# Kernel tuning notes

Measured on AMD Instinct MI355X. Metric: run time of the kernel, lower is better.

## Reference

```python
import jax, jax.numpy as jnp
import numpy as np

N = 50000      # nodes
E = 800000     # edges (before self-loops)
H = 4          # attention heads
C = 32         # out_features per head
DIN = 128      # in_features (== H*C so residual path is active)
ED = 16        # edge_dim
NEG = 0.2      # LeakyReLU negative slope (GATConv default)
EPS = 1e-5     # LayerNorm eps


def setup_inputs() -> dict:
    key = jax.random.key(0)
    ks = jax.random.split(key, 12)
    s = 0.05
    return {
        "x": jax.random.normal(ks[0], (N, DIN), dtype=jnp.float32),
        "edge_index": jax.random.randint(ks[1], (2, E), 0, N, dtype=jnp.int64),
        "edge_attr": jax.random.normal(ks[2], (E, ED), dtype=jnp.float32),
        # edge_processor: Linear(ED, ED) + ReLU (dropout = identity at eval)
        "W_ep": jax.random.normal(ks[3], (ED, ED), dtype=jnp.float32) * s,
        "b_ep": jnp.zeros((ED,), dtype=jnp.float32),
        # GATConv params (lin / lin_edge are bias-free in PyG)
        "W_lin": jax.random.normal(ks[4], (DIN, H * C), dtype=jnp.float32) * s,
        "W_edge": jax.random.normal(ks[5], (ED, H * C), dtype=jnp.float32) * s,
        "att_src": jax.random.normal(ks[6], (H, C), dtype=jnp.float32) * s,
        "att_dst": jax.random.normal(ks[7], (H, C), dtype=jnp.float32) * s,
        "att_edge": jax.random.normal(ks[8], (H, C), dtype=jnp.float32) * s,
        "bias": jnp.zeros((H * C,), dtype=jnp.float32),
        # LayerNorm params
        "ln_g": jnp.ones((H * C,), dtype=jnp.float32),
        "ln_b": jnp.zeros((H * C,), dtype=jnp.float32),
    }


def reference(x, edge_index, edge_attr, W_ep, b_ep, W_lin, W_edge,
              att_src, att_dst, att_edge, bias, ln_g, ln_b):
    n = x.shape[0]
    src, dst = edge_index[0], edge_index[1]

    # edge_processor: Linear + ReLU
    ea = jax.nn.relu(edge_attr @ W_ep + b_ep)                       # [E, ED]

    # add self-loops (PyG GATConv default), loop edge_attr = mean of incoming
    ones = jnp.ones((ea.shape[0],), dtype=ea.dtype)
    deg = jax.ops.segment_sum(ones, dst, num_segments=n)            # [N]
    loop_attr = jax.ops.segment_sum(ea, dst, num_segments=n)
    loop_attr = loop_attr / jnp.maximum(deg, 1.0)[:, None]          # [N, ED]
    loop = jnp.arange(n, dtype=src.dtype)
    src2 = jnp.concatenate([src, loop])                             # [E+N]
    dst2 = jnp.concatenate([dst, loop])
    ea2 = jnp.concatenate([ea, loop_attr], axis=0)                  # [E+N, ED]

    # node / edge linear transforms
    h = (x @ W_lin).reshape(n, H, C)                                # [N, H, C]
    a_src = jnp.einsum('nhc,hc->nh', h, att_src)                    # [N, H]
    a_dst = jnp.einsum('nhc,hc->nh', h, att_dst)
    e = (ea2 @ W_edge).reshape(-1, H, C)                            # [E+N, H, C]
    a_e = jnp.einsum('ehc,hc->eh', e, att_edge)                     # [E+N, H]

    # per-edge attention logits + leaky relu
    alpha = a_src[src2] + a_dst[dst2] + a_e                         # [E+N, H]
    alpha = jnp.where(alpha >= 0, alpha, NEG * alpha)

    # segment softmax over incoming edges of each dst node
    m = jax.ops.segment_max(alpha, dst2, num_segments=n)            # [N, H]
    ex = jnp.exp(alpha - m[dst2])
    denom = jax.ops.segment_sum(ex, dst2, num_segments=n)           # [N, H]
    w = ex / denom[dst2]                                            # [E+N, H]

    # scatter-aggregate messages
    msg = h[src2] * w[:, :, None]                                   # [E+N, H, C]
    out = jax.ops.segment_sum(msg, dst2, num_segments=n)            # [N, H, C]
    out = out.reshape(n, H * C) + bias

    # residual (DIN == H*C) + LayerNorm
    out = out + x
    mu = jnp.mean(out, axis=-1, keepdims=True)
    var = jnp.var(out, axis=-1, keepdims=True)
    out = (out - mu) * jax.lax.rsqrt(var + EPS) * ln_g + ln_b
    return out
```

## Files before the change

### kernel.cpp

```cpp
#include <hip/hip_runtime.h>
#include <hip/hip_fp16.h>
#include <math.h>

#define NN   50000
#define EE   800000
#define HH   4
#define CC   32
#define DINN 128
#define ED   16
#define NEGS 0.2f
#define LNEPS 1e-5f
#define SCAN_NB ((NN + 255) / 256)

struct __align__(16) Hp4 { __half2 a, b, c, d; };

__global__ __launch_bounds__(256, 3) void k_node(
        const float* __restrict__ x, const float* __restrict__ W_lin,
        const float* __restrict__ att_src, const float* __restrict__ att_dst,
        __half* __restrict__ hb, float* __restrict__ a_src, float* __restrict__ a_dst) {
    __shared__ float xr[64 * 132];
    int t = threadIdx.x;
    int row0 = blockIdx.x * 64;

    #pragma unroll
    for (int i = 0; i < 8; ++i) {
        int idx = t + 256 * i;
        int r = idx >> 5, kq = idx & 31;
        int row = row0 + r;
        float4 v = make_float4(0.f, 0.f, 0.f, 0.f);
        if (row < NN) v = ((const float4*)x)[(long)row * 32 + kq];
        *(float4*)&xr[r * 132 + kq * 4] = v;
    }
    __syncthreads();

    int colg = t & 15, rowg = t >> 4;
    int c0 = colg * 8;
    const float* Wp = W_lin + c0;
    float acc[4][8] = {};

    #pragma unroll 2
    for (int k = 0; k < DINN; k += 2) {
        float4 wa0 = *(const float4*)&Wp[(long)k * DINN];
        float4 wb0 = *(const float4*)&Wp[(long)k * DINN + 4];
        float4 wa1 = *(const float4*)&Wp[(long)(k + 1) * DINN];
        float4 wb1 = *(const float4*)&Wp[(long)(k + 1) * DINN + 4];
        #pragma unroll
        for (int i = 0; i < 4; ++i) {
            float2 xv = *(const float2*)&xr[(rowg * 4 + i) * 132 + k];
            acc[i][0] = fmaf(xv.x, wa0.x, acc[i][0]);
            acc[i][1] = fmaf(xv.x, wa0.y, acc[i][1]);
            acc[i][2] = fmaf(xv.x, wa0.z, acc[i][2]);
            acc[i][3] = fmaf(xv.x, wa0.w, acc[i][3]);
            acc[i][4] = fmaf(xv.x, wb0.x, acc[i][4]);
            acc[i][5] = fmaf(xv.x, wb0.y, acc[i][5]);
            acc[i][6] = fmaf(xv.x, wb0.z, acc[i][6]);
            acc[i][7] = fmaf(xv.x, wb0.w, acc[i][7]);
            acc[i][0] = fmaf(xv.y, wa1.x, acc[i][0]);
            acc[i][1] = fmaf(xv.y, wa1.y, acc[i][1]);
            acc[i][2] = fmaf(xv.y, wa1.z, acc[i][2]);
            acc[i][3] = fmaf(xv.y, wa1.w, acc[i][3]);
            acc[i][4] = fmaf(xv.y, wb1.x, acc[i][4]);
            acc[i][5] = fmaf(xv.y, wb1.y, acc[i][5]);
            acc[i][6] = fmaf(xv.y, wb1.z, acc[i][6]);
            acc[i][7] = fmaf(xv.y, wb1.w, acc[i][7]);
        }
    }

    int head = colg >> 2;
    int cw = c0 & 31;
    float4 as0 = *(const float4*)&att_src[head * CC + cw];
    float4 as1 = *(const float4*)&att_src[head * CC + cw + 4];
    float4 ad0 = *(const float4*)&att_dst[head * CC + cw];
    float4 ad1 = *(const float4*)&att_dst[head * CC + cw + 4];
    #pragma unroll
    for (int i = 0; i < 4; ++i) {
        int row = row0 + rowg * 4 + i;
        if (row < NN) {
            Hp4 p;
            p.a = __floats2half2_rn(acc[i][0], acc[i][1]);
            p.b = __floats2half2_rn(acc[i][2], acc[i][3]);
            p.c = __floats2half2_rn(acc[i][4], acc[i][5]);
            p.d = __floats2half2_rn(acc[i][6], acc[i][7]);
            *(Hp4*)&hb[(long)row * DINN + c0] = p;
        }
        float ps = acc[i][0]*as0.x + acc[i][1]*as0.y + acc[i][2]*as0.z + acc[i][3]*as0.w
                 + acc[i][4]*as1.x + acc[i][5]*as1.y + acc[i][6]*as1.z + acc[i][7]*as1.w;
        float pd = acc[i][0]*ad0.x + acc[i][1]*ad0.y + acc[i][2]*ad0.z + acc[i][3]*ad0.w
                 + acc[i][4]*ad1.x + acc[i][5]*ad1.y + acc[i][6]*ad1.z + acc[i][7]*ad1.w;
        ps += __shfl_xor(ps, 1); ps += __shfl_xor(ps, 2);
        pd += __shfl_xor(pd, 1); pd += __shfl_xor(pd, 2);
        if ((colg & 3) == 0 && row < NN) {
            a_src[row * 4 + head] = ps;
            a_dst[row * 4 + head] = pd;
        }
    }
}

__global__ __launch_bounds__(256) void k_count(const int* __restrict__ ei,
                                               int* __restrict__ cnt,
                                               int* __restrict__ rank) {
    int e = blockIdx.x * 256 + threadIdx.x;
    if (e < EE) rank[e] = atomicAdd(cnt + ei[EE + e], 1);
}

__global__ __launch_bounds__(256) void k_scanA(const int* __restrict__ cnt,
                                               int* __restrict__ partial) {
    int t = threadIdx.x, b = blockIdx.x;
    int i = b * 256 + t;
    int v = (i < NN) ? cnt[i] : 0;
    #pragma unroll
    for (int d = 1; d < 64; d <<= 1) v += __shfl_xor(v, d);
    __shared__ int wt[4];
    if ((t & 63) == 0) wt[t >> 6] = v;
    __syncthreads();
    if (t == 0) partial[b] = wt[0] + wt[1] + wt[2] + wt[3];
}

__global__ __launch_bounds__(256) void k_scanB(const int* __restrict__ partial,
                                               int* __restrict__ poff,
                                               int* __restrict__ row_start,
                                               const float* __restrict__ W_edge,
                                               const float* __restrict__ att_edge,
                                               float* __restrict__ v_edge) {
    int t = threadIdx.x;
    if (t < ED * HH) {
        int d = t >> 2, h = t & 3;
        float s = 0.f;
        for (int c = 0; c < CC; ++c)
            s += W_edge[d * (HH * CC) + h * CC + c] * att_edge[h * CC + c];
        v_edge[t] = s;
    }
    int lane = t & 63, w = t >> 6;
    int v = (t < SCAN_NB) ? partial[t] : 0;
    int sv = v;
    #pragma unroll
    for (int d = 1; d < 64; d <<= 1) {
        int o = __shfl_up(sv, d);
        if (lane >= d) sv += o;
    }
    __shared__ int wt[4];
    if (lane == 63) wt[w] = sv;
    __syncthreads();
    int base = 0;
    for (int j = 0; j < w; ++j) base += wt[j];
    if (t < SCAN_NB) poff[t] = base + sv - v;
    if (t == 255) row_start[NN] = wt[0] + wt[1] + wt[2] + wt[3];
}

__global__ __launch_bounds__(256) void k_scanC(const int* __restrict__ cnt,
                                               const int* __restrict__ poff,
                                               int* __restrict__ row_start) {
    int t = threadIdx.x, b = blockIdx.x;
    int i = b * 256 + t;
    int v = (i < NN) ? cnt[i] : 0;
    int lane = t & 63, w = t >> 6;
    int sv = v;
    #pragma unroll
    for (int d = 1; d < 64; d <<= 1) {
        int o = __shfl_up(sv, d);
        if (lane >= d) sv += o;
    }
    __shared__ int wt[4];
    if (lane == 63) wt[w] = sv;
    __syncthreads();
    int base = 0;
    for (int j = 0; j < w; ++j) base += wt[j];
    if (i < NN) row_start[i] = poff[b] + base + sv - v;
}

__global__ __launch_bounds__(256) void k_edge2(
        const int* __restrict__ ei, const float* __restrict__ edge_attr,
        const float* __restrict__ W_ep, const float* __restrict__ b_ep,
        const float* __restrict__ v_edge,
        const float* __restrict__ a_src, const float* __restrict__ a_dst,
        const int* __restrict__ row_start, const int* __restrict__ rank,
        uint4* __restrict__ pk, int* __restrict__ csr_src) {
    __shared__ float Wl[ED * ED];
    __shared__ float bl[ED];
    __shared__ float vl[ED * 4];
    int t = threadIdx.x;
    if (t < ED * ED) Wl[t] = W_ep[t];
    if (t < ED) bl[t] = b_ep[t];
    if (t < ED * 4) vl[t] = v_edge[t];
    __syncthreads();

    int e = blockIdx.x * 256 + t;
    if (e >= EE) return;

    float a[ED];
    const float4* ap = (const float4*)(edge_attr + (long)e * ED);
    float4 a0 = ap[0], a1 = ap[1], a2 = ap[2], a3 = ap[3];
    a[0]=a0.x; a[1]=a0.y; a[2]=a0.z; a[3]=a0.w;
    a[4]=a1.x; a[5]=a1.y; a[6]=a1.z; a[7]=a1.w;
    a[8]=a2.x; a[9]=a2.y; a[10]=a2.z; a[11]=a2.w;
    a[12]=a3.x; a[13]=a3.y; a[14]=a3.z; a[15]=a3.w;

    float r[ED];
    #pragma unroll
    for (int j = 0; j < ED; ++j) r[j] = bl[j];
    #pragma unroll
    for (int d = 0; d < ED; ++d) {
        float av = a[d];
        #pragma unroll
        for (int j = 0; j < ED; ++j) r[j] = fmaf(av, Wl[d * ED + j], r[j]);
    }

    float ae0 = 0.f, ae1 = 0.f, ae2 = 0.f, ae3 = 0.f;
    #pragma unroll
    for (int d = 0; d < ED; ++d) {
        float rd = fmaxf(r[d], 0.f);
        ae0 = fmaf(rd, vl[d * 4 + 0], ae0);
        ae1 = fmaf(rd, vl[d * 4 + 1], ae1);
        ae2 = fmaf(rd, vl[d * 4 + 2], ae2);
        ae3 = fmaf(rd, vl[d * 4 + 3], ae3);
    }

    int src = ei[e];
    int dst = ei[EE + e];
    float4 s4 = *(const float4*)&a_src[src * 4];
    float4 d4 = *(const float4*)&a_dst[dst * 4];
    float v0 = s4.x + d4.x + ae0;
    float v1 = s4.y + d4.y + ae1;
    float v2 = s4.z + d4.z + ae2;
    float v3 = s4.w + d4.w + ae3;
    v0 = (v0 >= 0.f) ? v0 : NEGS * v0;
    v1 = (v1 >= 0.f) ? v1 : NEGS * v1;
    v2 = (v2 >= 0.f) ? v2 : NEGS * v2;
    v3 = (v3 >= 0.f) ? v3 : NEGS * v3;

    __half2 p0 = __floats2half2_rn(__expf(v0), ae0);
    __half2 p1 = __floats2half2_rn(__expf(v1), ae1);
    __half2 p2 = __floats2half2_rn(__expf(v2), ae2);
    __half2 p3 = __floats2half2_rn(__expf(v3), ae3);
    int pos = row_start[dst] + rank[e];
    pk[pos] = make_uint4(*(unsigned*)&p0, *(unsigned*)&p1,
                         *(unsigned*)&p2, *(unsigned*)&p3);
    csr_src[pos] = src;
}

__global__ __launch_bounds__(256) void k_aggregate(
        const float* __restrict__ x, const __half2* __restrict__ hb,
        const float* __restrict__ a_src, const float* __restrict__ a_dst,
        const int* __restrict__ row_start,
        const unsigned* __restrict__ pkh, const int* __restrict__ srcs,
        const float* __restrict__ bias, const float* __restrict__ ln_g,
        const float* __restrict__ ln_b, float* __restrict__ out) {
    int t = threadIdx.x;
    int wave = t >> 6, lane = t & 63;
    int n = blockIdx.x * 4 + wave;
    if (n >= NN) return;

    int start = row_start[n];
    int deg   = row_start[n + 1] - start;
    int head  = lane >> 4;

    float accx = 0.f, accy = 0.f, s_own = 0.f, aes_own = 0.f;
    const unsigned* pp = pkh + (size_t)start * 4 + head;
    const int* sp = srcs + start;

    int k = 0;
    for (; k + 8 <= deg; k += 8) {
        unsigned pv[8]; int sv[8];
        #pragma unroll
        for (int j = 0; j < 8; ++j) {
            pv[j] = pp[(size_t)(k + j) * 4];
            sv[j] = sp[k + j];
        }
        __half2 hv[8];
        #pragma unroll
        for (int j = 0; j < 8; ++j) hv[j] = hb[(long)sv[j] * 64 + lane];
        #pragma unroll
        for (int j = 0; j < 8; ++j) {
            float2 wf = __half22float2(*(__half2*)&pv[j]);
            s_own += wf.x;
            aes_own += wf.y;
            float2 hf = __half22float2(hv[j]);
            accx = fmaf(wf.x, hf.x, accx);
            accy = fmaf(wf.x, hf.y, accy);
        }
    }
    for (; k < deg; ++k) {
        unsigned p = pp[(size_t)k * 4];
        int src = sp[k];
        __half2 hv = hb[(long)src * 64 + lane];
        float2 wf = __half22float2(*(__half2*)&p);
        s_own += wf.x;
        aes_own += wf.y;
        float2 hf = __half22float2(hv);
        accx = fmaf(wf.x, hf.x, accx);
        accy = fmaf(wf.x, hf.y, accy);
    }

    float inv_deg = 1.0f / fmaxf((float)deg, 1.0f);
    float v = a_src[n * 4 + head] + a_dst[n * 4 + head] + aes_own * inv_deg;
    v = (v >= 0.f) ? v : NEGS * v;
    float w0 = __expf(v);
    s_own += w0;
    float2 hn = __half22float2(hb[(long)n * 64 + lane]);
    accx = fmaf(w0, hn.x, accx);
    accy = fmaf(w0, hn.y, accy);
    float is = 1.0f / s_own;
    accx *= is; accy *= is;

    int c0 = lane * 2;
    float2 b2 = *(const float2*)&bias[c0];
    float2 x2 = *(const float2*)&x[(long)n * DINN + c0];
    float oa = accx + b2.x + x2.x;
    float ob = accy + b2.y + x2.y;
    float sum = oa + ob, sumsq = oa * oa + ob * ob;
    #pragma unroll
    for (int d2 = 1; d2 < 64; d2 <<= 1) {
        sum   += __shfl_xor(sum, d2);
        sumsq += __shfl_xor(sumsq, d2);
    }
    float mu  = sum * (1.0f / DINN);
    float var = sumsq * (1.0f / DINN) - mu * mu;
    float rs  = rsqrtf(var + LNEPS);
    float2 g2  = *(const float2*)&ln_g[c0];
    float2 lb2 = *(const float2*)&ln_b[c0];
    float2 o2;
    o2.x = (oa - mu) * rs * g2.x + lb2.x;
    o2.y = (ob - mu) * rs * g2.y + lb2.y;
    *(float2*)&out[(long)n * DINN + c0] = o2;
}

extern "C" void kernel_launch(void* const* d_in, const int* in_sizes, int n_in,
                              void* d_out, int out_size, void* d_ws, size_t ws_size,
                              hipStream_t stream) {
    const float* x         = (const float*)d_in[0];
    const int*   ei        = (const int*)d_in[1];
    const float* edge_attr = (const float*)d_in[2];
    const float* W_ep      = (const float*)d_in[3];
    const float* b_ep      = (const float*)d_in[4];
    const float* W_lin     = (const float*)d_in[5];
    const float* W_edge    = (const float*)d_in[6];
    const float* att_src   = (const float*)d_in[7];
    const float* att_dst   = (const float*)d_in[8];
    const float* att_edge  = (const float*)d_in[9];
    const float* bias      = (const float*)d_in[10];
    const float* ln_g      = (const float*)d_in[11];
    const float* ln_b      = (const float*)d_in[12];
    float* out = (float*)d_out;

    char* ws = (char*)d_ws;
    size_t o = 0;
    auto take = [&](size_t bytes) -> char* {
        char* p = ws + o;
        o = (o + bytes + 255) & ~(size_t)255;
        return p;
    };
    __half* hbuf      = (__half*)take((size_t)NN * DINN * 2);
    float*  a_src     = (float*)take((size_t)NN * 4 * 4);
    float*  a_dst     = (float*)take((size_t)NN * 4 * 4);
    float*  v_edge    = (float*)take((size_t)ED * 4 * 4);
    int*    cnt       = (int*)  take((size_t)NN * 4);
    int*    row_start = (int*)  take((size_t)(NN + 1) * 4);
    int*    rank      = (int*)  take((size_t)EE * 4);
    int*    partial   = (int*)  take((size_t)SCAN_NB * 4);
    int*    poff      = (int*)  take((size_t)SCAN_NB * 4);
    uint4*  pk        = (uint4*)take((size_t)EE * 16);
    int*    csr_src   = (int*)  take((size_t)EE * 4);

    hipMemsetAsync(cnt, 0, (size_t)NN * 4, stream);

    k_node<<<(NN + 63) / 64, 256, 0, stream>>>(x, W_lin, att_src, att_dst,
                                               hbuf, a_src, a_dst);
    k_count<<<(EE + 255) / 256, 256, 0, stream>>>(ei, cnt, rank);
    k_scanA<<<SCAN_NB, 256, 0, stream>>>(cnt, partial);
    k_scanB<<<1, 256, 0, stream>>>(partial, poff, row_start, W_edge, att_edge, v_edge);
    k_scanC<<<SCAN_NB, 256, 0, stream>>>(cnt, poff, row_start);
    k_edge2<<<(EE + 255) / 256, 256, 0, stream>>>(ei, edge_attr, W_ep, b_ep, v_edge,
                                                  a_src, a_dst, row_start, rank,
                                                  pk, csr_src);
    k_aggregate<<<(NN + 3) / 4, 256, 0, stream>>>(x, (const __half2*)hbuf,
                                                  a_src, a_dst, row_start,
                                                  (const unsigned*)pk, csr_src,
                                                  bias, ln_g, ln_b, out);
}
```

Baseline: 293.8 us.

## Fuse edge logit computation into counting pass, add lightweight CSR scatter kernel

Edge MLP and attention-logit computation move into the counting kernel, which writes a per-edge payload in edge order along with the atomic rank. A new light kernel then reads ei, rank and payload four edges per thread and scatters them into CSR order. The v_edge projection is recomputed per block instead of in the scan kernel. This adds a 12.8MB payload write and read round trip, but the previous version also re-read edge_attr and ei in the second pass. The gain hinges on whether the heavy compute now overlapping the atomics outweighs the extra traffic.

```diff
diff --git a/kernel.cpp b/kernel.cpp
--- a/kernel.cpp
+++ b/kernel.cpp
@@ -96,11 +96,83 @@
     }
 }
 
-__global__ __launch_bounds__(256) void k_count(const int* __restrict__ ei,
-                                               int* __restrict__ cnt,
-                                               int* __restrict__ rank) {
-    int e = blockIdx.x * 256 + threadIdx.x;
-    if (e < EE) rank[e] = atomicAdd(cnt + ei[EE + e], 1);
+__global__ __launch_bounds__(256) void k_edgeA(
+        const int* __restrict__ ei, const float* __restrict__ edge_attr,
+        const float* __restrict__ W_ep, const float* __restrict__ b_ep,
+        const float* __restrict__ W_edge, const float* __restrict__ att_edge,
+        const float* __restrict__ a_src, const float* __restrict__ a_dst,
+        int* __restrict__ cnt, int* __restrict__ rank,
+        uint4* __restrict__ payload) {
+    __shared__ float Wl[ED * ED];
+    __shared__ float bl[ED];
+    __shared__ float vl[ED * 4];
+    int t = threadIdx.x;
+    if (t < ED * ED) Wl[t] = W_ep[t];
+    if (t < ED) bl[t] = b_ep[t];
+    if (t >= 192 && t < 192 + 64) {
+        int q = t - 192;
+        int d = q >> 2, h = q & 3;
+        float s = 0.f;
+        #pragma unroll 8
+        for (int c = 0; c < CC; ++c)
+            s += W_edge[d * (HH * CC) + h * CC + c] * att_edge[h * CC + c];
+        vl[q] = s;
+    }
+    __syncthreads();
+
+    int e = blockIdx.x * 256 + t;
+    if (e >= EE) return;
+
+    int src = ei[e];
+    int dst = ei[EE + e];
+
+    float a[ED];
+    const float4* ap = (const float4*)(edge_attr + (long)e * ED);
+    float4 a0 = ap[0], a1 = ap[1], a2 = ap[2], a3 = ap[3];
+    a[0]=a0.x; a[1]=a0.y; a[2]=a0.z; a[3]=a0.w;
+    a[4]=a1.x; a[5]=a1.y; a[6]=a1.z; a[7]=a1.w;
+    a[8]=a2.x; a[9]=a2.y; a[10]=a2.z; a[11]=a2.w;
+    a[12]=a3.x; a[13]=a3.y; a[14]=a3.z; a[15]=a3.w;
+
+    float4 s4 = *(const float4*)&a_src[src * 4];
+    float4 d4 = *(const float4*)&a_dst[dst * 4];
+
+    float r[ED];
+    #pragma unroll
+    for (int j = 0; j < ED; ++j) r[j] = bl[j];
+    #pragma unroll
+    for (int d = 0; d < ED; ++d) {
+        float av = a[d];
+        #pragma unroll
+        for (int j = 0; j < ED; ++j) r[j] = fmaf(av, Wl[d * ED + j], r[j]);
+    }
+
+    float ae0 = 0.f, ae1 = 0.f, ae2 = 0.f, ae3 = 0.f;
+    #pragma unroll
+    for (int d = 0; d < ED; ++d) {
+        float rd = fmaxf(r[d], 0.f);
+        ae0 = fmaf(rd, vl[d * 4 + 0], ae0);
+        ae1 = fmaf(rd, vl[d * 4 + 1], ae1);
+        ae2 = fmaf(rd, vl[d * 4 + 2], ae2);
+        ae3 = fmaf(rd, vl[d * 4 + 3], ae3);
+    }
+
+    float v0 = s4.x + d4.x + ae0;
+    float v1 = s4.y + d4.y + ae1;
+    float v2 = s4.z + d4.z + ae2;
+    float v3 = s4.w + d4.w + ae3;
+    v0 = (v0 >= 0.f) ? v0 : NEGS * v0;
+    v1 = (v1 >= 0.f) ? v1 : NEGS * v1;
+    v2 = (v2 >= 0.f) ? v2 : NEGS * v2;
+    v3 = (v3 >= 0.f) ? v3 : NEGS * v3;
+
+    __half2 p0 = __floats2half2_rn(__expf(v0), ae0);
+    __half2 p1 = __floats2half2_rn(__expf(v1), ae1);
+    __half2 p2 = __floats2half2_rn(__expf(v2), ae2);
+    __half2 p3 = __floats2half2_rn(__expf(v3), ae3);
+    payload[e] = make_uint4(*(unsigned*)&p0, *(unsigned*)&p1,
+                            *(unsigned*)&p2, *(unsigned*)&p3);
+    rank[e] = atomicAdd(cnt + dst, 1);
 }
 
 __global__ __launch_bounds__(256) void k_scanA(const int* __restrict__ cnt,
@@ -118,18 +190,8 @@
 
 __global__ __launch_bounds__(256) void k_scanB(const int* __restrict__ partial,
                                                int* __restrict__ poff,
-                                               int* __restrict__ row_start,
-                                               const float* __restrict__ W_edge,
-                                               const float* __restrict__ att_edge,
-                                               float* __restrict__ v_edge) {
+                                               int* __restrict__ row_start) {
     int t = threadIdx.x;
-    if (t < ED * HH) {
-        int d = t >> 2, h = t & 3;
-        float s = 0.f;
-        for (int c = 0; c < CC; ++c)
-            s += W_edge[d * (HH * CC) + h * CC + c] * att_edge[h * CC + c];
-        v_edge[t] = s;
-    }
     int lane = t & 63, w = t >> 6;
     int v = (t < SCAN_NB) ? partial[t] : 0;
     int sv = v;
@@ -168,74 +230,31 @@
     if (i < NN) row_start[i] = poff[b] + base + sv - v;
 }
 
-__global__ __launch_bounds__(256) void k_edge2(
-        const int* __restrict__ ei, const float* __restrict__ edge_attr,
-        const float* __restrict__ W_ep, const float* __restrict__ b_ep,
-        const float* __restrict__ v_edge,
-        const float* __restrict__ a_src, const float* __restrict__ a_dst,
-        const int* __restrict__ row_start, const int* __restrict__ rank,
+__global__ __launch_bounds__(256) void k_edgeB(
+        const int* __restrict__ ei, const uint4* __restrict__ payload,
+        const int* __restrict__ rank, const int* __restrict__ row_start,
         uint4* __restrict__ pk, int* __restrict__ csr_src) {
-    __shared__ float Wl[ED * ED];
-    __shared__ float bl[ED];
-    __shared__ float vl[ED * 4];
-    int t = threadIdx.x;
-    if (t < ED * ED) Wl[t] = W_ep[t];
-    if (t < ED) bl[t] = b_ep[t];
-    if (t < ED * 4) vl[t] = v_edge[t];
-    __syncthreads();
-
-    int e = blockIdx.x * 256 + t;
-    if (e >= EE) return;
-
-    float a[ED];
-    const float4* ap = (const float4*)(edge_attr + (long)e * ED);
-    float4 a0 = ap[0], a1 = ap[1], a2 = ap[2], a3 = ap[3];
-    a[0]=a0.x; a[1]=a0.y; a[2]=a0.z; a[3]=a0.w;
-    a[4]=a1.x; a[5]=a1.y; a[6]=a1.z; a[7]=a1.w;
-    a[8]=a2.x; a[9]=a2.y; a[10]=a2.z; a[11]=a2.w;
-    a[12]=a3.x; a[13]=a3.y; a[14]=a3.z; a[15]=a3.w;
-
-    float r[ED];
-    #pragma unroll
-    for (int j = 0; j < ED; ++j) r[j] = bl[j];
-    #pragma unroll
-    for (int d = 0; d < ED; ++d) {
-        float av = a[d];
-        #pragma unroll
-        for (int j = 0; j < ED; ++j) r[j] = fmaf(av, Wl[d * ED + j], r[j]);
-    }
-
-    float ae0 = 0.f, ae1 = 0.f, ae2 = 0.f, ae3 = 0.f;
-    #pragma unroll
-    for (int d = 0; d < ED; ++d) {
-        float rd = fmaxf(r[d], 0.f);
-        ae0 = fmaf(rd, vl[d * 4 + 0], ae0);
-        ae1 = fmaf(rd, vl[d * 4 + 1], ae1);
-        ae2 = fmaf(rd, vl[d * 4 + 2], ae2);
-        ae3 = fmaf(rd, vl[d * 4 + 3], ae3);
-    }
-
-    int src = ei[e];
-    int dst = ei[EE + e];
-    float4 s4 = *(const float4*)&a_src[src * 4];
-    float4 d4 = *(const float4*)&a_dst[dst * 4];
-    float v0 = s4.x + d4.x + ae0;
-    float v1 = s4.y + d4.y + ae1;
-    float v2 = s4.z + d4.z + ae2;
-    float v3 = s4.w + d4.w + ae3;
-    v0 = (v0 >= 0.f) ? v0 : NEGS * v0;
-    v1 = (v1 >= 0.f) ? v1 : NEGS * v1;
-    v2 = (v2 >= 0.f) ? v2 : NEGS * v2;
-    v3 = (v3 >= 0.f) ? v3 : NEGS * v3;
-
-    __half2 p0 = __floats2half2_rn(__expf(v0), ae0);
-    __half2 p1 = __floats2half2_rn(__expf(v1), ae1);
-    __half2 p2 = __floats2half2_rn(__expf(v2), ae2);
-    __half2 p3 = __floats2half2_rn(__expf(v3), ae3);
-    int pos = row_start[dst] + rank[e];
-    pk[pos] = make_uint4(*(unsigned*)&p0, *(unsigned*)&p1,
-                         *(unsigned*)&p2, *(unsigned*)&p3);
-    csr_src[pos] = src;
+    int base = (blockIdx.x * 256 + threadIdx.x) * 4;
+    if (base + 3 < EE) {
+        int4 s4 = *(const int4*)(ei + base);
+        int4 d4 = *(const int4*)(ei + EE + base);
+        int4 r4 = *(const int4*)(rank + base);
+        uint4 p0 = payload[base], p1 = payload[base + 1];
+        uint4 p2 = payload[base + 2], p3 = payload[base + 3];
+        int q0 = row_start[d4.x] + r4.x;
+        int q1 = row_start[d4.y] + r4.y;
+        int q2 = row_start[d4.z] + r4.z;
+        int q3 = row_start[d4.w] + r4.w;
+        pk[q0] = p0; pk[q1] = p1; pk[q2] = p2; pk[q3] = p3;
+        csr_src[q0] = s4.x; csr_src[q1] = s4.y;
+        csr_src[q2] = s4.z; csr_src[q3] = s4.w;
+    } else {
+        for (int e = base; e < EE; ++e) {
+            int q = row_start[ei[EE + e]] + rank[e];
+            pk[q] = payload[e];
+            csr_src[q] = ei[e];
+        }
+    }
 }
 
 __global__ __launch_bounds__(256) void k_aggregate(
@@ -352,12 +371,12 @@
     __half* hbuf      = (__half*)take((size_t)NN * DINN * 2);
     float*  a_src     = (float*)take((size_t)NN * 4 * 4);
     float*  a_dst     = (float*)take((size_t)NN * 4 * 4);
-    float*  v_edge    = (float*)take((size_t)ED * 4 * 4);
     int*    cnt       = (int*)  take((size_t)NN * 4);
     int*    row_start = (int*)  take((size_t)(NN + 1) * 4);
     int*    rank      = (int*)  take((size_t)EE * 4);
     int*    partial   = (int*)  take((size_t)SCAN_NB * 4);
     int*    poff      = (int*)  take((size_t)SCAN_NB * 4);
+    uint4*  payload   = (uint4*)take((size_t)EE * 16);
     uint4*  pk        = (uint4*)take((size_t)EE * 16);
     int*    csr_src   = (int*)  take((size_t)EE * 4);
 
@@ -365,13 +384,14 @@
 
     k_node<<<(NN + 63) / 64, 256, 0, stream>>>(x, W_lin, att_src, att_dst,
                                                hbuf, a_src, a_dst);
-    k_count<<<(EE + 255) / 256, 256, 0, stream>>>(ei, cnt, rank);
+    k_edgeA<<<(EE + 255) / 256, 256, 0, stream>>>(ei, edge_attr, W_ep, b_ep,
+                                                  W_edge, att_edge, a_src, a_dst,
+                                                  cnt, rank, payload);
     k_scanA<<<SCAN_NB, 256, 0, stream>>>(cnt, partial);
-    k_scanB<<<1, 256, 0, stream>>>(partial, poff, row_start, W_edge, att_edge, v_edge);
+    k_scanB<<<1, 256, 0, stream>>>(partial, poff, row_start);
     k_scanC<<<SCAN_NB, 256, 0, stream>>>(cnt, poff, row_start);
-    k_edge2<<<(EE + 255) / 256, 256, 0, stream>>>(ei, edge_attr, W_ep, b_ep, v_edge,
-                                                  a_src, a_dst, row_start, rank,
-                                                  pk, csr_src);
+    k_edgeB<<<(EE / 4 + 255) / 256, 256, 0, stream>>>(ei, payload, rank,
+                                                      row_start, pk, csr_src);
     k_aggregate<<<(NN + 3) / 4, 256, 0, stream>>>(x, (const __half2*)hbuf,
                                                   a_src, a_dst, row_start,
                                                   (const unsigned*)pk, csr_src,
```

Result: faster. 284.5 us (-3.2%).
